# Performance work log

Hardware: AMD Instinct MI355X
Metric: run time of the kernel (lower is better)

## Reference

```python
import jax, jax.numpy as jnp
import numpy as np

V, D, F, H, NB, S, B = 16384, 512, 2048, 8, 4, 512, 2
T_STEPS = 3      # config.T: number of PC inference iterations
GAMMA = 0.1      # state-update step size


def _layernorm(x, s, b):
    m = x.mean(-1, keepdims=True)
    v = ((x - m) ** 2).mean(-1, keepdims=True)
    return (x - m) * jax.lax.rsqrt(v + 1e-5) * s + b


def setup_inputs() -> dict:
    key = jax.random.key(0)
    ks = jax.random.split(key, 12)
    r = lambda k, sh: jax.random.normal(k, sh, jnp.float32) * 0.02
    return {
        'word_emb': r(ks[0], (V, D)),
        'pos_emb': r(ks[1], (S, D)),
        'Wq': r(ks[2], (NB, D, D)),
        'Wk': r(ks[3], (NB, D, D)),
        'Wv': r(ks[4], (NB, D, D)),
        'bq': jnp.zeros((NB, D), jnp.float32),
        'bk': jnp.zeros((NB, D), jnp.float32),
        'bv': jnp.zeros((NB, D), jnp.float32),
        'Wo': r(ks[5], (NB, D, D)),
        'bo': jnp.zeros((NB, D), jnp.float32),
        'ln1_s': jnp.ones((NB, D), jnp.float32),
        'ln1_b': jnp.zeros((NB, D), jnp.float32),
        'ln2_s': jnp.ones((NB, D), jnp.float32),
        'ln2_b': jnp.zeros((NB, D), jnp.float32),
        'W1': r(ks[6], (NB, D, F)),
        'b1': jnp.zeros((NB, F), jnp.float32),
        'W2': r(ks[7], (NB, F, D)),
        'b2': jnp.zeros((NB, D), jnp.float32),
        'Wout': r(ks[8], (D, V)),
        'bout': jnp.zeros((V,), jnp.float32),
        'input_ids': jax.random.randint(ks[9], (B, S), 0, V),
        'target_ids': jax.random.randint(ks[10], (B, S), 0, V),
    }


def _forward(word_emb, pos_emb, Wq, Wk, Wv, bq, bk, bv, Wo, bo,
             ln1_s, ln1_b, ln2_s, ln2_b, W1, b1, W2, b2, Wout, bout,
             input_ids, target_ids):
    Bsz, Sl = input_ids.shape
    dh = D // H
    scale = 1.0 / float(np.sqrt(dh))
    ids = jnp.clip(input_ids, 0, V - 1)
    target = jax.nn.one_hot(jnp.clip(target_ids, 0, V - 1), V, dtype=word_emb.dtype)
    # bottom prediction: word + position embeddings
    mu_emb = word_emb[ids] + pos_emb[jnp.arange(Sl)][None]  # (B,S,D)
    causal = jnp.tril(jnp.ones((Sl, Sl), bool))
    neg = jnp.finfo(word_emb.dtype).min

    def attn(x, b):
        h = _layernorm(x, ln1_s[b], ln1_b[b])
        q = (h @ Wq[b] + bq[b]).reshape(Bsz, Sl, H, dh)
        k = (h @ Wk[b] + bk[b]).reshape(Bsz, Sl, H, dh)
        v = (h @ Wv[b] + bv[b]).reshape(Bsz, Sl, H, dh)
        sc = jnp.einsum('bqhd,bkhd->bhqk', q, k) * scale
        sc = jnp.where(causal, sc, neg)
        a = jax.nn.softmax(sc, axis=-1)
        return jnp.einsum('bhqk,bkhd->bqhd', a, v).reshape(Bsz, Sl, D)

    # generative functions g[l]: x_l -> mu_{l+1}; 4 PC layers per block
    # (pc_qkv->attn ctx, pc_output->Wo, pc_layer1->gelu(fc1), pc_layer2->fc2)
    gs = []
    for b in range(NB):
        gs.append(lambda x, b=b: attn(x, b))
        gs.append(lambda x, b=b: x @ Wo[b] + bo[b])
        gs.append(lambda x, b=b: jax.nn.gelu(_layernorm(x, ln2_s[b], ln2_b[b]) @ W1[b] + b1[b]))
        gs.append(lambda x, b=b: x @ W2[b] + b2[b])
    g_top = lambda x: x @ Wout + bout  # output pc layer -> logits mu

    # init_x: forward sweep sets each latent to its prediction
    xs = [mu_emb]
    for g in gs:
        xs.append(g(xs[-1]))
    L = len(gs)

    # T-step iterative PC inference: eps_l = x_l - mu_l, top clamped to target
    # x_l <- x_l + GAMMA * (J_{g_l}(x_l)^T eps_{l+1} - eps_l)
    for _ in range(T_STEPS):
        preds, vjps = [], []
        for l in range(L):
            mu, vj = jax.vjp(gs[l], xs[l])
            preds.append(mu)
            vjps.append(vj)
        logits, vj_top = jax.vjp(g_top, xs[L])
        eps = [xs[0] - mu_emb] + [xs[l + 1] - preds[l] for l in range(L)]
        eps_top = logits - target
        new_xs = []
        for l in range(L + 1):
            td = vjps[l](eps[l + 1])[0] if l < L else vj_top(eps_top)[0]
            new_xs.append(xs[l] + GAMMA * (td - eps[l]))
        xs = new_xs

    return g_top(xs[L])  # get_mu('linear_output')


def reference(word_emb, pos_emb, Wq, Wk, Wv, bq, bk, bv, Wo, bo,
              ln1_s, ln1_b, ln2_s, ln2_b, W1, b1, W2, b2, Wout, bout,
              input_ids, target_ids):
    return _forward(word_emb, pos_emb, Wq, Wk, Wv, bq, bk, bv, Wo, bo,
                    ln1_s, ln1_b, ln2_s, ln2_b, W1, b1, W2, b2, Wout, bout,
                    input_ids, target_ids)
```

## Files before the change

kernel.cpp:

```cpp
#include <hip/hip_runtime.h>
#include <hip/hip_bf16.h>
#include <math.h>

#define D_   512
#define F_   2048
#define V_   16384
#define H_   8
#define DH_  64
#define S_   512
#define B_   2
#define M_   1024
#define MD_  (M_ * D_)
#define MF_  (M_ * F_)
#define GAMMA_ 0.1f

typedef unsigned int u32;
typedef unsigned short u16;
typedef __attribute__((ext_vector_type(4))) float f32x4;
typedef __attribute__((ext_vector_type(8))) short s16x8;
typedef __attribute__((ext_vector_type(4))) u16 u16x4;
typedef __attribute__((ext_vector_type(8))) u16 u16x8;

__device__ __forceinline__ u16 f2b(float f) {
    __hip_bfloat16 h = __float2bfloat16(f);
    return *reinterpret_cast<u16*>(&h);
}
__device__ __forceinline__ float b2f(u16 v) {
    u32 u = ((u32)v) << 16;
    float f; __builtin_memcpy(&f, &u, 4); return f;
}
__device__ __forceinline__ u16x4 pack4(f32x4 v) {
    u16x4 o; o.x = f2b(v[0]); o.y = f2b(v[1]); o.z = f2b(v[2]); o.w = f2b(v[3]);
    return o;
}

__device__ __forceinline__ void gl_lds16(const void* g, void* l) {
    __builtin_amdgcn_global_load_lds((const __attribute__((address_space(1))) u32*)g,
                                     (__attribute__((address_space(3))) u32*)l, 16, 0, 0);
}

__device__ __forceinline__ float gelu_f(float v) {
    float u = 0.7978845608028654f * (v + 0.044715f * v * v * v);
    return 0.5f * v * (1.f + tanhf(u));
}

__device__ __forceinline__ f32x4 xpose4(f32x4 v, int b) {
#pragma unroll
    for (int s = 1; s < 4; s <<= 1) {
        f32x4 nv;
#pragma unroll
        for (int j = 0; j < 4; ++j) {
            float ex = __shfl_xor(v[j ^ s], s, 64);
            nv[j] = ((b ^ j) & s) ? ex : v[j];
        }
        v = nv;
    }
    return v;
}

__device__ __forceinline__ float wave_sum(float v) {
#pragma unroll
    for (int o = 32; o > 0; o >>= 1) v += __shfl_xor(v, o, 64);
    return v;
}

#define E_F32   0
#define E_GELU  1
#define E_TD    2
#define E_EC2   3
#define E_QKV3  4
#define E_OUT   5
#define E_BF16  6

template<int BK>
__device__ __forceinline__ int swz(int c, int row) {
    if constexpr (BK == 32) return c ^ ((row >> 1) & 3);
    else                    return c ^ (row & 7);
}

template<int BM, int BN, int BK, int FM, int FN, int EPI>
__global__ __launch_bounds__(256)
void mfma_gemm(const u16* __restrict__ A, const u16* __restrict__ B,
               float* __restrict__ Cf, u16* __restrict__ Cb,
               u16* __restrict__ Cb2, u16* __restrict__ Cb3,
               const float* __restrict__ bias,
               int K, int lda, int ldb, int ldc,
               long sC, long sKz, float alpha,
               const float* __restrict__ base, const float* __restrict__ subv,
               const float* __restrict__ cvec, const u16* __restrict__ woutTb,
               const int* __restrict__ tcl,
               float* __restrict__ ebF, u16* __restrict__ ebB)
{
    constexpr int WC = BN / (FN * 16);
    static_assert((BM / (FM * 16)) * WC == 4, "4 waves");
    constexpr int LPR = BK / 8;
    constexpr int RPI = 2048 / BK;
    __shared__ __align__(16) u16 Asl[2][BM * BK];
    __shared__ __align__(16) u16 Bsl[2][BN * BK];
    const int t = threadIdx.x, l = t & 63, wid = t >> 6;
    const int m0 = blockIdx.y * BM, n0 = blockIdx.x * BN;
    const long z = blockIdx.z;
    A += z * sKz;
    B += z * sKz;
    if (Cf) Cf += z * sC;

    f32x4 acc[FM][FN] = {};
    const int rm = (wid / WC) * (FM * 16), cn = (wid % WC) * (FN * 16);
    const int lr = l & 15, hi = l >> 4;
    const int srl = t / LPR, sc = t % LPR;

    auto stage = [&](int k0, int pb) {
#pragma unroll
        for (int i = 0; i < BM / RPI; ++i) {
            int row = i * RPI + srl;
            gl_lds16(A + (size_t)(m0 + row) * lda + k0 + swz<BK>(sc, row) * 8,
                     &Asl[pb][i * 2048 + t * 8]);
        }
#pragma unroll
        for (int i = 0; i < BN / RPI; ++i) {
            int row = i * RPI + srl;
            gl_lds16(B + (size_t)(n0 + row) * ldb + k0 + swz<BK>(sc, row) * 8,
                     &Bsl[pb][i * 2048 + t * 8]);
        }
    };
    auto compute = [&](int pb) {
#pragma unroll
        for (int kk = 0; kk < BK / 32; ++kk) {
            s16x8 av[FM], bv[FN];
#pragma unroll
            for (int fm = 0; fm < FM; ++fm)
                av[fm] = *(const s16x8*)&Asl[pb][(rm + fm * 16 + lr) * BK + swz<BK>(kk * 4 + hi, lr) * 8];
#pragma unroll
            for (int fn = 0; fn < FN; ++fn)
                bv[fn] = *(const s16x8*)&Bsl[pb][(cn + fn * 16 + lr) * BK + swz<BK>(kk * 4 + hi, lr) * 8];
#pragma unroll
            for (int fm = 0; fm < FM; ++fm)
#pragma unroll
                for (int fn = 0; fn < FN; ++fn)
                    acc[fm][fn] = __builtin_amdgcn_mfma_f32_16x16x32_bf16(av[fm], bv[fn], acc[fm][fn], 0, 0, 0);
        }
    };

    stage(0, 0);
    __syncthreads();
    int cur = 0;
    for (int k0 = BK; k0 < K; k0 += BK) {
        stage(k0, cur ^ 1);
        compute(cur);
        __syncthreads();
        cur ^= 1;
    }
    compute(cur);

    const int qb = lr & 3, qi = lr >> 2;
#pragma unroll
    for (int fm = 0; fm < FM; ++fm)
#pragma unroll
        for (int fn = 0; fn < FN; ++fn) {
            const int gm = m0 + rm + fm * 16 + hi * 4 + qb;
            const int gn0 = n0 + cn + fn * 16 + qi * 4;
            const size_t idx0 = (size_t)gm * ldc + gn0;
            if constexpr (EPI == E_QKV3) {
                const int gnf = n0 + cn + fn * 16;
                const int sel = gnf >> 9;
                if (sel < 2) {
                    f32x4 v = xpose4(acc[fm][fn], qb);
                    f32x4 bv4 = *(const f32x4*)&bias[gn0];
#pragma unroll
                    for (int j = 0; j < 4; ++j) v[j] += bv4[j];
                    int b = gm >> 9, s = gm & (S_ - 1);
                    int d9 = gn0 & 511, h = d9 >> 6, d = d9 & 63;
                    u16* dst = (sel == 0) ? Cb : Cb2;
                    *(u16x4*)&dst[(((size_t)(b * H_ + h) * S_ + s) << 6) + d] = pack4(v);
                } else {
                    const int gnl = gnf + lr;
                    const int gm0 = m0 + rm + fm * 16 + hi * 4;
                    int b = gm0 >> 9, s0 = gm0 & (S_ - 1);
                    int d9 = gnl & 511, h = d9 >> 6, d = d9 & 63;
                    float bb = bias[gnl];
                    f32x4 v = acc[fm][fn];
#pragma unroll
                    for (int j = 0; j < 4; ++j) v[j] += bb;
                    *(u16x4*)&Cb3[((((size_t)(b * H_ + h)) << 6) + d) * S_ + s0] = pack4(v);
                }
            } else {
                f32x4 v = xpose4(acc[fm][fn], qb);
                if constexpr (EPI == E_F32) {
#pragma unroll
                    for (int j = 0; j < 4; ++j) v[j] *= alpha;
                    if (bias) {
                        f32x4 bv4 = *(const f32x4*)&bias[gn0];
#pragma unroll
                        for (int j = 0; j < 4; ++j) v[j] += bv4[j];
                    }
                    *(f32x4*)&Cf[idx0] = v;
                    if (Cb) *(u16x4*)&Cb[idx0] = pack4(v);
                } else if constexpr (EPI == E_OUT) {
                    f32x4 bv4 = *(const f32x4*)&bias[gn0];
#pragma unroll
                    for (int j = 0; j < 4; ++j) v[j] += bv4[j];
                    *(f32x4*)&Cf[idx0] = v;
                } else if constexpr (EPI == E_GELU) {
                    f32x4 bv4 = *(const f32x4*)&bias[gn0];
#pragma unroll
                    for (int j = 0; j < 4; ++j) v[j] = gelu_f(v[j] + bv4[j]);
                    *(u16x4*)&Cb[idx0] = pack4(v);
                } else if constexpr (EPI == E_TD) {
                    const int tc = tcl[gm];
                    f32x4 cv4 = *(const f32x4*)&cvec[gn0];
                    f32x4 ba4 = *(const f32x4*)&base[idx0];
                    u16x4 gv = *(const u16x4*)&woutTb[(size_t)tc * D_ + gn0];
                    f32x4 dlt, o2;
#pragma unroll
                    for (int j = 0; j < 4; ++j)
                        dlt[j] = GAMMA_ * (v[j] + cv4[j] - b2f(gv[j]));
                    if (subv) {
                        f32x4 sv4 = *(const f32x4*)&subv[idx0];
#pragma unroll
                        for (int j = 0; j < 4; ++j) dlt[j] -= GAMMA_ * sv4[j];
                    }
#pragma unroll
                    for (int j = 0; j < 4; ++j) o2[j] = ba4[j] + dlt[j];
                    if (Cf) *(f32x4*)&Cf[idx0] = o2;
                    *(u16x4*)&Cb[idx0] = pack4(o2);
                    if (ebF) *(f32x4*)&ebF[idx0] = dlt;
                    if (ebB) *(u16x4*)&ebB[idx0] = pack4(dlt);
                } else if constexpr (EPI == E_EC2) {
                    f32x4 ba4 = *(const f32x4*)&base[idx0];
                    f32x4 sv4 = *(const f32x4*)&subv[idx0];
#pragma unroll
                    for (int j = 0; j < 4; ++j) v[j] = ba4[j] - sv4[j] - GAMMA_ * v[j];
                    *(f32x4*)&Cf[idx0] = v;
                } else if constexpr (EPI == E_BF16) {
                    *(u16x4*)&Cb[idx0] = pack4(v);
                }
            }
        }
}

__global__ __launch_bounds__(256)
void flash_attn(const u16* __restrict__ q, const u16* __restrict__ k,
                const u16* __restrict__ vT, u16* __restrict__ ctx)
{
    __shared__ __align__(16) u16 Ks[2][64 * 64];
    __shared__ __align__(16) u16 Vs[2][64 * 64];
    __shared__ __align__(16) u16 Ps[4][16 * 64];
    const int t = threadIdx.x, l = t & 63, w = t >> 6;
    const int qt = blockIdx.x, z = blockIdx.y;
    const int bb = z >> 3, hh = z & 7;
    const int lr = l & 15, hi = l >> 4;
    const u16* qp = q + (((size_t)z * S_ + qt * 64 + w * 16) << 6);
    const u16* kp = k + ((size_t)z * S_ << 6);
    const u16* vp = vT + (((size_t)z) << 6) * S_;

    const s16x8 aq0 = *(const s16x8*)&qp[lr * 64 + hi * 8];
    const s16x8 aq1 = *(const s16x8*)&qp[lr * 64 + 32 + hi * 8];

    f32x4 o[4] = {};
    float m[4], ls[4];
#pragma unroll
    for (int r = 0; r < 4; ++r) { m[r] = -3.0e38f; ls[r] = 0.f; }
    const int qrow = qt * 64 + w * 16 + hi * 4;
    const int srow = t >> 3, scl = t & 7;
    const int cg1 = (scl ^ (srow & 7)) * 8;
    const int srow2 = srow + 32;
    const int cg2 = (scl ^ (srow2 & 7)) * 8;
    const int sw7 = (lr & 7);

    auto stage = [&](int j, int pb) {
        gl_lds16(kp + ((size_t)(j * 64 + srow) << 6) + cg1, &Ks[pb][t * 8]);
        gl_lds16(vp + (size_t)srow * S_ + j * 64 + cg1, &Vs[pb][t * 8]);
        gl_lds16(kp + ((size_t)(j * 64 + srow2) << 6) + cg2, &Ks[pb][(t + 256) * 8]);
        gl_lds16(vp + (size_t)srow2 * S_ + j * 64 + cg2, &Vs[pb][(t + 256) * 8]);
    };

    stage(0, 0);
    __syncthreads();
    int cur = 0;
    for (int j = 0; j <= qt; ++j) {
        if (j < qt) stage(j + 1, cur ^ 1);

        float pv[4][4];
#pragma unroll
        for (int fn = 0; fn < 4; ++fn) {
            f32x4 acc = {};
            acc = __builtin_amdgcn_mfma_f32_16x16x32_bf16(aq0,
                    *(const s16x8*)&Ks[cur][((fn * 16 + lr) << 6) + ((hi ^ sw7) * 8)], acc, 0, 0, 0);
            acc = __builtin_amdgcn_mfma_f32_16x16x32_bf16(aq1,
                    *(const s16x8*)&Ks[cur][((fn * 16 + lr) << 6) + (((hi + 4) ^ sw7) * 8)], acc, 0, 0, 0);
#pragma unroll
            for (int r = 0; r < 4; ++r) pv[fn][r] = acc[r] * 0.125f;
        }
        if (j == qt) {
#pragma unroll
            for (int fn = 0; fn < 4; ++fn) {
                int col = j * 64 + fn * 16 + lr;
#pragma unroll
                for (int r = 0; r < 4; ++r)
                    if (col > qrow + r) pv[fn][r] = -3.0e38f;
            }
        }
        float sc[4], rs[4];
#pragma unroll
        for (int r = 0; r < 4; ++r) {
            float x = fmaxf(fmaxf(pv[0][r], pv[1][r]), fmaxf(pv[2][r], pv[3][r]));
#pragma unroll
            for (int off = 1; off < 16; off <<= 1) x = fmaxf(x, __shfl_xor(x, off, 64));
            float nm = fmaxf(m[r], x);
            sc[r] = expf(m[r] - nm);
            m[r] = nm;
            rs[r] = 0.f;
        }
#pragma unroll
        for (int fn = 0; fn < 4; ++fn)
#pragma unroll
            for (int r = 0; r < 4; ++r) {
                float p = expf(pv[fn][r] - m[r]);
                pv[fn][r] = p;
                rs[r] += p;
            }
#pragma unroll
        for (int r = 0; r < 4; ++r) {
#pragma unroll
            for (int off = 1; off < 16; off <<= 1) rs[r] += __shfl_xor(rs[r], off, 64);
            ls[r] = ls[r] * sc[r] + rs[r];
        }
#pragma unroll
        for (int fn = 0; fn < 4; ++fn)
#pragma unroll
            for (int r = 0; r < 4; ++r) o[fn][r] *= sc[r];
#pragma unroll
        for (int fn = 0; fn < 4; ++fn)
#pragma unroll
            for (int r = 0; r < 4; ++r) {
                int qr = hi * 4 + r;
                int ci = (2 * fn + (lr >> 3)) ^ (qr & 7);
                Ps[w][qr * 64 + ci * 8 + (lr & 7)] = f2b(pv[fn][r]);
            }
#pragma unroll
        for (int ks = 0; ks < 2; ++ks) {
            const s16x8 pa = *(const s16x8*)&Ps[w][lr * 64 + (((4 * ks + hi) ^ sw7) * 8)];
#pragma unroll
            for (int fn = 0; fn < 4; ++fn)
                o[fn] = __builtin_amdgcn_mfma_f32_16x16x32_bf16(pa,
                        *(const s16x8*)&Vs[cur][((fn * 16 + lr) << 6) + (((hi + 4 * ks) ^ sw7) * 8)], o[fn], 0, 0, 0);
        }
        __syncthreads();
        cur ^= 1;
    }
    float inv[4];
#pragma unroll
    for (int r = 0; r < 4; ++r) inv[r] = 1.f / ls[r];
    u16* cp = ctx + ((size_t)(bb * S_ + qt * 64 + w * 16) * D_) + hh * 64;
    const int qb = lr & 3, qi = lr >> 2;
#pragma unroll
    for (int fn = 0; fn < 4; ++fn) {
        f32x4 v = o[fn];
#pragma unroll
        for (int r = 0; r < 4; ++r) v[r] *= inv[r];
        v = xpose4(v, qb);
        *(u16x4*)&cp[(size_t)(hi * 4 + qb) * D_ + fn * 16 + qi * 4] = pack4(v);
    }
}

__global__ __launch_bounds__(256)
void prep0(const float* __restrict__ bq, const float* __restrict__ bk,
           const float* __restrict__ bv, const int* __restrict__ target_ids,
           float* __restrict__ qkvb, int* __restrict__ tcl, float* __restrict__ cvec)
{
    int i = blockIdx.x * 256 + threadIdx.x;
    if (i < 512) cvec[i] = 0.f;
    else if (i < 1536) {
        int mm = i - 512;
        int v = target_ids[mm];
        tcl[mm] = v < 0 ? 0 : (v > V_ - 1 ? V_ - 1 : v);
    } else if (i < 1536 + 6144) {
        int j = i - 1536;
        int b = j / 1536, r = j - b * 1536;
        qkvb[j] = (r < 512) ? bq[b * 512 + r]
                : (r < 1024) ? bk[b * 512 + r - 512] : bv[b * 512 + r - 1024];
    }
}

__global__ __launch_bounds__(256)
void mega_prep(const float* __restrict__ Wq, const float* __restrict__ Wk,
               const float* __restrict__ Wv, const float* __restrict__ Wo,
               const float* __restrict__ W1, const float* __restrict__ W2,
               const float* __restrict__ Wout, const float* __restrict__ bout,
               u16* __restrict__ wqkvT, u16* __restrict__ woT, u16* __restrict__ w1T,
               u16* __restrict__ w2T, u16* __restrict__ woutT,
               u16* __restrict__ woutD, float* __restrict__ cvec)
{
    __shared__ float tile[64][65];
    const int g = blockIdx.x, t = threadIdx.x;

    const float* in = nullptr;
    u16 *outT = nullptr, *outC = nullptr;
    int R = 512, C = 512, tx = 0, ty = 0;
    bool doCvec = false;

    if (g < 768) {
        int sel = g / 256, rem = g % 256, zz = rem >> 6, tl = rem & 63;
        in = (sel == 0 ? Wq : sel == 1 ? Wk : Wv) + (size_t)zz * 262144;
        outT = wqkvT + (size_t)zz * 786432 + sel * 262144;
        tx = tl & 7; ty = tl >> 3;
    } else if (g < 1024) {
        int rem = g - 768, zz = rem >> 6, tl = rem & 63;
        in = Wo + (size_t)zz * 262144; outT = woT + (size_t)zz * 262144;
        tx = tl & 7; ty = tl >> 3;
    } else if (g < 2048) {
        int rem = g - 1024, zz = rem >> 8, tl = rem & 255;
        in = W1 + (size_t)zz * 1048576; outT = w1T + (size_t)zz * 1048576;
        C = 2048; tx = tl & 31; ty = tl >> 5;
    } else if (g < 3072) {
        int rem = g - 2048, zz = rem >> 8, tl = rem & 255;
        in = W2 + (size_t)zz * 1048576; outT = w2T + (size_t)zz * 1048576;
        R = 2048; tx = tl & 7; ty = tl >> 3;
    } else {
        int tl = g - 3072;
        in = Wout; outT = woutT; outC = woutD; doCvec = true;
        C = 16384; tx = tl & 255; ty = tl >> 8;
    }

    const int r0 = ty * 64, c0 = tx * 64;
#pragma unroll
    for (int p = 0; p < 4; ++p) {
        int row = p * 16 + (t >> 4), col = (t & 15) * 4;
        float4 v = *(const float4*)&in[(size_t)(r0 + row) * C + c0 + col];
        tile[row][col] = v.x; tile[row][col + 1] = v.y;
        tile[row][col + 2] = v.z; tile[row][col + 3] = v.w;
        if (outC) {
            f32x4 fv; fv[0] = v.x; fv[1] = v.y; fv[2] = v.z; fv[3] = v.w;
            *(u16x4*)&outC[(size_t)(r0 + row) * C + c0 + col] = pack4(fv);
        }
    }
    __syncthreads();
#pragma unroll
    for (int p = 0; p < 2; ++p) {
        int orow = p * 32 + (t >> 3), oc = (t & 7) * 8;
        u16x8 o;
#pragma unroll
        for (int j = 0; j < 8; ++j) o[j] = f2b(tile[oc + j][orow]);
        *(u16x8*)&outT[(size_t)(c0 + orow) * R + r0 + oc] = o;
    }
    if (doCvec) {
        int r = t >> 2, q = t & 3;
        float s = 0.f;
#pragma unroll
        for (int i = 0; i < 16; ++i)
            s += tile[r][q * 16 + i] * bout[c0 + q * 16 + i];
        s += __shfl_xor(s, 1, 64);
        s += __shfl_xor(s, 2, 64);
        if (q == 0) atomicAdd(&cvec[r0 + r], s);
    }
}

__global__ void gred_kernel(const float* __restrict__ P, u16* __restrict__ G)
{
    int i = blockIdx.x * blockDim.x + threadIdx.x;
    if (i < D_ * D_) {
        float s = 0.f;
#pragma unroll
        for (int zz = 0; zz < 16; ++zz) s += P[(size_t)zz * D_ * D_ + i];
        G[i] = f2b(s);
    }
}

__global__ void embed_kernel(const float4* __restrict__ we, const float4* __restrict__ pe,
                             const int* __restrict__ ids, float4* __restrict__ o)
{
    int t = blockIdx.x * blockDim.x + threadIdx.x;
    int d4 = t & 127, row = t >> 7;
    int ss = row & (S_ - 1);
    int id = ids[row];
    id = id < 0 ? 0 : (id > V_ - 1 ? V_ - 1 : id);
    float4 a = we[(size_t)id * 128 + d4];
    float4 b = pe[(size_t)ss * 128 + d4];
    o[(size_t)row * 128 + d4] = make_float4(a.x + b.x, a.y + b.y, a.z + b.z, a.w + b.w);
}

__global__ __launch_bounds__(256)
void ln_fwd_kernel(const float* __restrict__ x, const float* __restrict__ s,
                   const float* __restrict__ bb, u16* __restrict__ h)
{
    const int l = threadIdx.x & 63, w = threadIdx.x >> 6;
    const int row = blockIdx.x * 4 + w;
    const float* xr = x + (size_t)row * D_;
    const int c0 = l * 8;
    float4 a = *(const float4*)&xr[c0];
    float4 b = *(const float4*)&xr[c0 + 4];
    float sum = a.x + a.y + a.z + a.w + b.x + b.y + b.z + b.w;
    float mu = wave_sum(sum) * (1.f / D_);
    float d0 = a.x - mu, d1 = a.y - mu, d2 = a.z - mu, d3 = a.w - mu;
    float d4 = b.x - mu, d5 = b.y - mu, d6 = b.z - mu, d7 = b.w - mu;
    float vs = d0*d0 + d1*d1 + d2*d2 + d3*d3 + d4*d4 + d5*d5 + d6*d6 + d7*d7;
    float var = wave_sum(vs) * (1.f / D_);
    float r = rsqrtf(var + 1e-5f);
    float4 s0 = *(const float4*)&s[c0], s1 = *(const float4*)&s[c0 + 4];
    float4 b0 = *(const float4*)&bb[c0], b1 = *(const float4*)&bb[c0 + 4];
    u16* hr = h + (size_t)row * D_;
    f32x4 o0, o1;
    o0[0] = d0 * r * s0.x + b0.x; o0[1] = d1 * r * s0.y + b0.y;
    o0[2] = d2 * r * s0.z + b0.z; o0[3] = d3 * r * s0.w + b0.w;
    o1[0] = d4 * r * s1.x + b1.x; o1[1] = d5 * r * s1.y + b1.y;
    o1[2] = d6 * r * s1.z + b1.z; o1[3] = d7 * r * s1.w + b1.w;
    *(u16x4*)&hr[c0] = pack4(o0);
    *(u16x4*)&hr[c0 + 4] = pack4(o1);
}

extern "C" void kernel_launch(void* const* d_in, const int* in_sizes, int n_in,
                              void* d_out, int out_size, void* d_ws, size_t ws_size,
                              hipStream_t stream)
{
    (void)in_sizes; (void)n_in; (void)out_size;
    const float* Wq  = (const float*)d_in[2];
    const float* Wk  = (const float*)d_in[3];
    const float* Wv  = (const float*)d_in[4];
    const float* bq  = (const float*)d_in[5];
    const float* bk  = (const float*)d_in[6];
    const float* bv  = (const float*)d_in[7];
    const float* Wo  = (const float*)d_in[8];
    const float* bo  = (const float*)d_in[9];
    const float* ln1_s = (const float*)d_in[10];
    const float* ln1_b = (const float*)d_in[11];
    const float* ln2_s = (const float*)d_in[12];
    const float* ln2_b = (const float*)d_in[13];
    const float* W1  = (const float*)d_in[14];
    const float* b1  = (const float*)d_in[15];
    const float* W2  = (const float*)d_in[16];
    const float* b2  = (const float*)d_in[17];
    const float* Wout = (const float*)d_in[18];
    const float* bout = (const float*)d_in[19];
    const int* input_ids  = (const int*)d_in[20];
    const int* target_ids = (const int*)d_in[21];
    float* out = (float*)d_out;

    char* wsb = (char*)d_ws;
    size_t off = 0;
    auto alloc = [&](size_t bytes) -> void* {
        off = (off + 255) & ~(size_t)255;
        void* p = wsb + off; off += bytes; return p;
    };
    u16* wqkvT = (u16*)alloc((size_t)4 * 1536 * D_ * 2);
    u16* woT   = (u16*)alloc((size_t)4 * D_ * D_ * 2);
    u16* w1T   = (u16*)alloc((size_t)4 * D_ * F_ * 2);
    u16* w2T   = (u16*)alloc((size_t)4 * D_ * F_ * 2);
    u16* woutT = (u16*)alloc((size_t)V_ * D_ * 2);
    u16* G_b   = (u16*)alloc((size_t)D_ * D_ * 2);
    u16* H2_b  = (u16*)alloc((size_t)D_ * D_ * 2);
    float* qkvb = (float*)alloc((size_t)4 * 1536 * 4);
    float* bufB = (float*)alloc((size_t)MD_ * 4);
    u16* h_b    = (u16*)alloc((size_t)MD_ * 2);
    u16* gelu_b = (u16*)alloc((size_t)MF_ * 2);
    u16* x16_b  = (u16*)alloc((size_t)MD_ * 2);
    float* cvec = (float*)alloc(D_ * 4);
    int* tcl    = (int*)alloc(M_ * 4);
    size_t uStart = (off + 255) & ~(size_t)255;
    off = uStart;
    u16* woutD   = (u16*)alloc((size_t)V_ * D_ * 2);
    float* Gpart = (float*)alloc((size_t)16 * D_ * D_ * 4);
    size_t endG = off;
    off = uStart;
    u16* q_b   = (u16*)alloc((size_t)MD_ * 2);
    u16* k_b   = (u16*)alloc((size_t)MD_ * 2);
    u16* v_b   = (u16*)alloc((size_t)MD_ * 2);
    u16* ctx_b = (u16*)alloc((size_t)MD_ * 2);
    size_t endA = off;
    off = uStart;
    float* xA  = (float*)alloc((size_t)MD_ * 4);
    float* xB  = (float*)alloc((size_t)MD_ * 4);
    float* eb  = (float*)alloc((size_t)MD_ * 4);
    float* ec  = (float*)alloc((size_t)MD_ * 4);
    u16* xA_b  = (u16*)alloc((size_t)MD_ * 2);
    u16* xB_b  = (u16*)alloc((size_t)MD_ * 2);
    u16* xC_b  = (u16*)alloc((size_t)MD_ * 2);
    u16* eb_b  = (u16*)alloc((size_t)MD_ * 2);
    size_t endT = off;
    size_t need = endG > endA ? endG : endA;
    if (endT > need) need = endT;
    if (need > ws_size) return;

    dim3 blk(256);
    const long NL = 0;
    #define GZ nullptr, nullptr, nullptr, nullptr, nullptr, nullptr, nullptr

    prep0<<<dim3(32), blk, 0, stream>>>(bq, bk, bv, target_ids, qkvb, tcl, cvec);
    mega_prep<<<dim3(5120), blk, 0, stream>>>(Wq, Wk, Wv, Wo, W1, W2, Wout, bout,
        wqkvT, woT, w1T, w2T, woutT, woutD, cvec);
    mfma_gemm<128, 128, 64, 4, 4, E_F32><<<dim3(4, 4, 16), blk, 0, stream>>>(
        woutD, woutD, Gpart, nullptr, nullptr, nullptr, nullptr, 1024, V_, V_, D_,
        (long)D_ * D_, 1024, 1.f, GZ);
    gred_kernel<<<dim3(1024), blk, 0, stream>>>(Gpart, G_b);
    mfma_gemm<64, 64, 128, 2, 2, E_BF16><<<dim3(8, 8, 1), blk, 0, stream>>>(
        w2T + (size_t)3 * D_ * F_, w2T + (size_t)3 * D_ * F_, nullptr, H2_b,
        nullptr, nullptr, nullptr, F_, F_, F_, D_, NL, NL, 1.f, GZ);

    embed_kernel<<<dim3(512), blk, 0, stream>>>((const float4*)d_in[0], (const float4*)d_in[1],
                                                input_ids, (float4*)bufB);
    for (int b = 0; b < 4; ++b) {
        const size_t wDD = (size_t)b * D_ * D_, wDF = (size_t)b * D_ * F_;
        ln_fwd_kernel<<<dim3(M_ / 4), blk, 0, stream>>>(bufB, ln1_s + b * D_, ln1_b + b * D_, h_b);
        mfma_gemm<128, 64, 128, 4, 2, E_QKV3><<<dim3(24, 8, 1), blk, 0, stream>>>(
            h_b, wqkvT + (size_t)b * 1536 * 512, nullptr, q_b, k_b, v_b,
            qkvb + b * 1536, D_, D_, D_, 0, NL, NL, 1.f, GZ);
        flash_attn<<<dim3(8, 16), blk, 0, stream>>>(q_b, k_b, v_b, ctx_b);
        mfma_gemm<64, 64, 128, 2, 2, E_F32><<<dim3(8, 16, 1), blk, 0, stream>>>(
            ctx_b, woT + wDD, bufB, nullptr, nullptr, nullptr, bo + b * D_,
            D_, D_, D_, D_, NL, NL, 1.f, GZ);
        ln_fwd_kernel<<<dim3(M_ / 4), blk, 0, stream>>>(bufB, ln2_s + b * D_, ln2_b + b * D_, h_b);
        mfma_gemm<64, 64, 128, 2, 2, E_GELU><<<dim3(32, 16, 1), blk, 0, stream>>>(
            h_b, w1T + wDF, nullptr, gelu_b, nullptr, nullptr, b1 + b * F_,
            D_, D_, D_, F_, NL, NL, 1.f, GZ);
        mfma_gemm<64, 64, 128, 2, 2, E_F32><<<dim3(8, 16, 1), blk, 0, stream>>>(
            gelu_b, w2T + wDF, bufB, (b == 3) ? x16_b : nullptr, nullptr, nullptr, b2 + b * D_,
            F_, F_, F_, D_, NL, NL, 1.f, GZ);
    }

    mfma_gemm<64, 64, 128, 2, 2, E_TD><<<dim3(8, 16, 1), blk, 0, stream>>>(
        x16_b, G_b, xA, xA_b, nullptr, nullptr, nullptr, D_, D_, D_, D_, NL, NL, 1.f,
        bufB, nullptr, cvec, woutT, tcl, eb, eb_b);
    mfma_gemm<64, 64, 128, 2, 2, E_TD><<<dim3(8, 16, 1), blk, 0, stream>>>(
        xA_b, G_b, xB, xB_b, nullptr, nullptr, nullptr, D_, D_, D_, D_, NL, NL, 1.f,
        xA, eb, cvec, woutT, tcl, nullptr, nullptr);
    mfma_gemm<64, 64, 128, 2, 2, E_EC2><<<dim3(8, 16, 1), blk, 0, stream>>>(
        eb_b, H2_b, ec, nullptr, nullptr, nullptr, nullptr, D_, D_, D_, D_, NL, NL, 1.f,
        xB, bufB, nullptr, nullptr, nullptr, nullptr, nullptr);
    mfma_gemm<64, 64, 128, 2, 2, E_TD><<<dim3(8, 16, 1), blk, 0, stream>>>(
        xB_b, G_b, nullptr, xC_b, nullptr, nullptr, nullptr, D_, D_, D_, D_, NL, NL, 1.f,
        xB, ec, cvec, woutT, tcl, nullptr, nullptr);
    mfma_gemm<128, 256, 64, 4, 8, E_OUT><<<dim3(64, 8, 1), blk, 0, stream>>>(
        xC_b, woutT, out, nullptr, nullptr, nullptr, bout, D_, D_, D_, V_, NL, NL, 1.f, GZ);
    #undef GZ
}
```

Before: 435.1 us.

## Triple-buffer LDS staging with vmcnt waits in GEMM and flash attention

Replaces the double-buffered global-to-LDS pipeline in the MFMA GEMM and flash-attention kernels with a three-stage ring. Two tiles are now kept in flight, with `s_waitcnt vmcnt` on outstanding loads and a single barrier per iteration instead of two. To keep shared memory in check, the K tile size is halved for most GEMM launches (128→64, and 64→32 for the output projection). The intent is to hide more global-load latency behind MFMA work, at the cost of more loop iterations and barriers per GEMM and higher LDS use per block.

```diff
diff --git a/kernel.cpp b/kernel.cpp
--- a/kernel.cpp
+++ b/kernel.cpp
@@ -95,8 +95,9 @@
     static_assert((BM / (FM * 16)) * WC == 4, "4 waves");
     constexpr int LPR = BK / 8;
     constexpr int RPI = 2048 / BK;
-    __shared__ __align__(16) u16 Asl[2][BM * BK];
-    __shared__ __align__(16) u16 Bsl[2][BN * BK];
+    constexpr int NISS = BM / RPI + BN / RPI;
+    __shared__ __align__(16) u16 Asl[3][BM * BK];
+    __shared__ __align__(16) u16 Bsl[3][BN * BK];
     const int t = threadIdx.x, l = t & 63, wid = t >> 6;
     const int m0 = blockIdx.y * BM, n0 = blockIdx.x * BN;
     const long z = blockIdx.z;
@@ -141,16 +142,22 @@
         }
     };
 
+    const int nst = K / BK;
     stage(0, 0);
-    __syncthreads();
-    int cur = 0;
-    for (int k0 = BK; k0 < K; k0 += BK) {
-        stage(k0, cur ^ 1);
-        compute(cur);
-        __syncthreads();
-        cur ^= 1;
-    }
-    compute(cur);
+    if (nst > 1) stage(BK, 1);
+    int rd = 0, wr = 2;
+    for (int s = 0; s < nst; ++s) {
+        if (s < nst - 1)
+            asm volatile("s_waitcnt vmcnt(%0)" :: "i"(NISS) : "memory");
+        else
+            asm volatile("s_waitcnt vmcnt(0)" ::: "memory");
+        __builtin_amdgcn_s_barrier();
+        __builtin_amdgcn_sched_barrier(0);
+        compute(rd);
+        if (s + 2 < nst) stage((s + 2) * BK, wr);
+        rd = (rd + 1 == 3) ? 0 : rd + 1;
+        wr = (wr + 1 == 3) ? 0 : wr + 1;
+    }
 
     const int qb = lr & 3, qi = lr >> 2;
 #pragma unroll
@@ -242,8 +249,8 @@
 void flash_attn(const u16* __restrict__ q, const u16* __restrict__ k,
                 const u16* __restrict__ vT, u16* __restrict__ ctx)
 {
-    __shared__ __align__(16) u16 Ks[2][64 * 64];
-    __shared__ __align__(16) u16 Vs[2][64 * 64];
+    __shared__ __align__(16) u16 Ks[3][64 * 64];
+    __shared__ __align__(16) u16 Vs[3][64 * 64];
     __shared__ __align__(16) u16 Ps[4][16 * 64];
     const int t = threadIdx.x, l = t & 63, w = t >> 6;
     const int qt = blockIdx.x, z = blockIdx.y;
@@ -275,19 +282,22 @@
     };
 
     stage(0, 0);
-    __syncthreads();
-    int cur = 0;
+    if (qt > 0) stage(1, 1);
+    int rd = 0, wr = 2;
     for (int j = 0; j <= qt; ++j) {
-        if (j < qt) stage(j + 1, cur ^ 1);
+        if (j < qt) asm volatile("s_waitcnt vmcnt(4)" ::: "memory");
+        else        asm volatile("s_waitcnt vmcnt(0)" ::: "memory");
+        __builtin_amdgcn_s_barrier();
+        __builtin_amdgcn_sched_barrier(0);
 
         float pv[4][4];
 #pragma unroll
         for (int fn = 0; fn < 4; ++fn) {
             f32x4 acc = {};
             acc = __builtin_amdgcn_mfma_f32_16x16x32_bf16(aq0,
-                    *(const s16x8*)&Ks[cur][((fn * 16 + lr) << 6) + ((hi ^ sw7) * 8)], acc, 0, 0, 0);
+                    *(const s16x8*)&Ks[rd][((fn * 16 + lr) << 6) + ((hi ^ sw7) * 8)], acc, 0, 0, 0);
             acc = __builtin_amdgcn_mfma_f32_16x16x32_bf16(aq1,
-                    *(const s16x8*)&Ks[cur][((fn * 16 + lr) << 6) + (((hi + 4) ^ sw7) * 8)], acc, 0, 0, 0);
+                    *(const s16x8*)&Ks[rd][((fn * 16 + lr) << 6) + (((hi + 4) ^ sw7) * 8)], acc, 0, 0, 0);
 #pragma unroll
             for (int r = 0; r < 4; ++r) pv[fn][r] = acc[r] * 0.125f;
         }
@@ -343,10 +353,11 @@
 #pragma unroll
             for (int fn = 0; fn < 4; ++fn)
                 o[fn] = __builtin_amdgcn_mfma_f32_16x16x32_bf16(pa,
-                        *(const s16x8*)&Vs[cur][((fn * 16 + lr) << 6) + (((hi + 4 * ks) ^ sw7) * 8)], o[fn], 0, 0, 0);
-        }
-        __syncthreads();
-        cur ^= 1;
+                        *(const s16x8*)&Vs[rd][((fn * 16 + lr) << 6) + (((hi + 4 * ks) ^ sw7) * 8)], o[fn], 0, 0, 0);
+        }
+        if (j + 2 <= qt) stage(j + 2, wr);
+        rd = (rd + 1 == 3) ? 0 : rd + 1;
+        wr = (wr + 1 == 3) ? 0 : wr + 1;
     }
     float inv[4];
 #pragma unroll
@@ -444,14 +455,14 @@
         *(u16x8*)&outT[(size_t)(c0 + orow) * R + r0 + oc] = o;
     }
     if (doCvec) {
-        int r = t >> 2, q = t & 3;
+        int r = t >> 2, qq = t & 3;
         float s = 0.f;
 #pragma unroll
         for (int i = 0; i < 16; ++i)
-            s += tile[r][q * 16 + i] * bout[c0 + q * 16 + i];
+            s += tile[r][qq * 16 + i] * bout[c0 + qq * 16 + i];
         s += __shfl_xor(s, 1, 64);
         s += __shfl_xor(s, 2, 64);
-        if (q == 0) atomicAdd(&cvec[r0 + r], s);
+        if (qq == 0) atomicAdd(&cvec[r0 + r], s);
     }
 }
 
@@ -591,7 +602,7 @@
         woutD, woutD, Gpart, nullptr, nullptr, nullptr, nullptr, 1024, V_, V_, D_,
         (long)D_ * D_, 1024, 1.f, GZ);
     gred_kernel<<<dim3(1024), blk, 0, stream>>>(Gpart, G_b);
-    mfma_gemm<64, 64, 128, 2, 2, E_BF16><<<dim3(8, 8, 1), blk, 0, stream>>>(
+    mfma_gemm<64, 64, 64, 2, 2, E_BF16><<<dim3(8, 8, 1), blk, 0, stream>>>(
         w2T + (size_t)3 * D_ * F_, w2T + (size_t)3 * D_ * F_, nullptr, H2_b,
         nullptr, nullptr, nullptr, F_, F_, F_, D_, NL, NL, 1.f, GZ);
 
@@ -600,35 +611,35 @@
     for (int b = 0; b < 4; ++b) {
         const size_t wDD = (size_t)b * D_ * D_, wDF = (size_t)b * D_ * F_;
         ln_fwd_kernel<<<dim3(M_ / 4), blk, 0, stream>>>(bufB, ln1_s + b * D_, ln1_b + b * D_, h_b);
-        mfma_gemm<128, 64, 128, 4, 2, E_QKV3><<<dim3(24, 8, 1), blk, 0, stream>>>(
+        mfma_gemm<128, 64, 64, 4, 2, E_QKV3><<<dim3(24, 8, 1), blk, 0, stream>>>(
             h_b, wqkvT + (size_t)b * 1536 * 512, nullptr, q_b, k_b, v_b,
             qkvb + b * 1536, D_, D_, D_, 0, NL, NL, 1.f, GZ);
         flash_attn<<<dim3(8, 16), blk, 0, stream>>>(q_b, k_b, v_b, ctx_b);
-        mfma_gemm<64, 64, 128, 2, 2, E_F32><<<dim3(8, 16, 1), blk, 0, stream>>>(
+        mfma_gemm<64, 64, 64, 2, 2, E_F32><<<dim3(8, 16, 1), blk, 0, stream>>>(
             ctx_b, woT + wDD, bufB, nullptr, nullptr, nullptr, bo + b * D_,
             D_, D_, D_, D_, NL, NL, 1.f, GZ);
         ln_fwd_kernel<<<dim3(M_ / 4), blk, 0, stream>>>(bufB, ln2_s + b * D_, ln2_b + b * D_, h_b);
-        mfma_gemm<64, 64, 128, 2, 2, E_GELU><<<dim3(32, 16, 1), blk, 0, stream>>>(
+        mfma_gemm<64, 64, 64, 2, 2, E_GELU><<<dim3(32, 16, 1), blk, 0, stream>>>(
             h_b, w1T + wDF, nullptr, gelu_b, nullptr, nullptr, b1 + b * F_,
             D_, D_, D_, F_, NL, NL, 1.f, GZ);
-        mfma_gemm<64, 64, 128, 2, 2, E_F32><<<dim3(8, 16, 1), blk, 0, stream>>>(
+        mfma_gemm<64, 64, 64, 2, 2, E_F32><<<dim3(8, 16, 1), blk, 0, stream>>>(
             gelu_b, w2T + wDF, bufB, (b == 3) ? x16_b : nullptr, nullptr, nullptr, b2 + b * D_,
             F_, F_, F_, D_, NL, NL, 1.f, GZ);
     }
 
-    mfma_gemm<64, 64, 128, 2, 2, E_TD><<<dim3(8, 16, 1), blk, 0, stream>>>(
+    mfma_gemm<64, 64, 64, 2, 2, E_TD><<<dim3(8, 16, 1), blk, 0, stream>>>(
         x16_b, G_b, xA, xA_b, nullptr, nullptr, nullptr, D_, D_, D_, D_, NL, NL, 1.f,
         bufB, nullptr, cvec, woutT, tcl, eb, eb_b);
-    mfma_gemm<64, 64, 128, 2, 2, E_TD><<<dim3(8, 16, 1), blk, 0, stream>>>(
+    mfma_gemm<64, 64, 64, 2, 2, E_TD><<<dim3(8, 16, 1), blk, 0, stream>>>(
         xA_b, G_b, xB, xB_b, nullptr, nullptr, nullptr, D_, D_, D_, D_, NL, NL, 1.f,
         xA, eb, cvec, woutT, tcl, nullptr, nullptr);
-    mfma_gemm<64, 64, 128, 2, 2, E_EC2><<<dim3(8, 16, 1), blk, 0, stream>>>(
+    mfma_gemm<64, 64, 64, 2, 2, E_EC2><<<dim3(8, 16, 1), blk, 0, stream>>>(
         eb_b, H2_b, ec, nullptr, nullptr, nullptr, nullptr, D_, D_, D_, D_, NL, NL, 1.f,
         xB, bufB, nullptr, nullptr, nullptr, nullptr, nullptr);
-    mfma_gemm<64, 64, 128, 2, 2, E_TD><<<dim3(8, 16, 1), blk, 0, stream>>>(
+    mfma_gemm<64, 64, 64, 2, 2, E_TD><<<dim3(8, 16, 1), blk, 0, stream>>>(
         xB_b, G_b, nullptr, xC_b, nullptr, nullptr, nullptr, D_, D_, D_, D_, NL, NL, 1.f,
         xB, ec, cvec, woutT, tcl, nullptr, nullptr);
-    mfma_gemm<128, 256, 64, 4, 8, E_OUT><<<dim3(64, 8, 1), blk, 0, stream>>>(
+    mfma_gemm<128, 256, 32, 4, 8, E_OUT><<<dim3(64, 8, 1), blk, 0, stream>>>(
         xC_b, woutT, out, nullptr, nullptr, nullptr, bout, D_, D_, D_, V_, NL, NL, 1.f, GZ);
     #undef GZ
 }
```

New measurement: 423.8 us. 2.6% less time.
